# Optimization experiments

Hardware: AMD Instinct MI355X
Metric: run time of the kernel (lower is better)

## Reference

```python
import jax, jax.numpy as jnp
import numpy as np

D1 = 512
D2 = 1024  # = 2*D1 (concat of x1,y1 along channels)
B, S = 4, 2048


def _self_attn(x, Wq, bq, Wk, bk, Wv, bv):
    # Linear layers use torch convention: out = x @ W.T + b
    q = jnp.einsum('bsd,ed->bse', x, Wq) + bq
    k = jnp.einsum('bsd,ed->bse', x, Wk) + bk
    v = jnp.einsum('bsd,ed->bse', x, Wv) + bv
    # NOTE: original module has no 1/sqrt(d) scaling — keep it faithful.
    scores = jnp.einsum('bqe,bke->bqk', q, k)  # [B,S,S]
    attn = jax.nn.softmax(scores, axis=-1)
    return jnp.einsum('bqk,bke->bqe', attn, v)


def setup_inputs() -> dict:
    key = jax.random.key(0)
    ks = jax.random.split(key, 18)
    s1 = 1.0 / np.sqrt(D1)
    s2 = 1.0 / np.sqrt(D2)
    return {
        'x': jax.random.normal(ks[0], (B, S, D1), jnp.float32),
        'y': jax.random.normal(ks[1], (B, S, D1), jnp.float32),
        'sa1_Wq': jax.random.normal(ks[2], (D1, D1), jnp.float32) * s1,
        'sa1_bq': jnp.zeros((D1,), jnp.float32),
        'sa1_Wk': jax.random.normal(ks[3], (D1, D1), jnp.float32) * s1,
        'sa1_bk': jnp.zeros((D1,), jnp.float32),
        'sa1_Wv': jax.random.normal(ks[4], (D1, D1), jnp.float32) * s1,
        'sa1_bv': jnp.zeros((D1,), jnp.float32),
        'sa2_Wq': jax.random.normal(ks[5], (D2, D2), jnp.float32) * s2,
        'sa2_bq': jnp.zeros((D2,), jnp.float32),
        'sa2_Wk': jax.random.normal(ks[6], (D2, D2), jnp.float32) * s2,
        'sa2_bk': jnp.zeros((D2,), jnp.float32),
        'sa2_Wv': jax.random.normal(ks[7], (D2, D2), jnp.float32) * s2,
        'sa2_bv': jnp.zeros((D2,), jnp.float32),
        'weight1': jnp.ones((1,), jnp.float32),
        'weight2': jnp.ones((1,), jnp.float32),
    }


def reference(x, y, sa1_Wq, sa1_bq, sa1_Wk, sa1_bk, sa1_Wv, sa1_bv,
              sa2_Wq, sa2_bq, sa2_Wk, sa2_bk, sa2_Wv, sa2_bv,
              weight1, weight2):
    x1 = _self_attn(x, sa1_Wq, sa1_bq, sa1_Wk, sa1_bk, sa1_Wv, sa1_bv)
    x1 = x1 + y * weight2
    y1 = _self_attn(y, sa1_Wq, sa1_bq, sa1_Wk, sa1_bk, sa1_Wv, sa1_bv)
    y1 = y1 + x * weight1
    temp = jnp.concatenate((x1, y1), axis=2)  # [B,S,2*D1]
    return _self_attn(temp, sa2_Wq, sa2_bq, sa2_Wk, sa2_bk, sa2_Wv, sa2_bv)
```

## Files before the change

### kernel.cpp

```cpp
#include <hip/hip_runtime.h>
#include <hip/hip_bf16.h>
#include <cstdint>
#include <cstddef>


typedef __bf16 bf16;
typedef __attribute__((ext_vector_type(8))) __bf16 bf16x8;
typedef __attribute__((ext_vector_type(4))) __bf16 bf16x4;
typedef __attribute__((ext_vector_type(4))) float f32x4;

__device__ __forceinline__ void gld16(const bf16* g, bf16* s) {
    __builtin_amdgcn_global_load_lds(
        (const __attribute__((address_space(1))) void*)g,
        (__attribute__((address_space(3))) void*)s, 16, 0, 0);
}

#define WAIT_VM8   __builtin_amdgcn_s_waitcnt(8 | (7 << 4) | (0xF << 8))
#define WAIT_VM0   __builtin_amdgcn_s_waitcnt(0 | (7 << 4) | (0xF << 8))
#define WAIT_LGKM0 __builtin_amdgcn_s_waitcnt(0xF | (7 << 4) | (0 << 8) | (3 << 14))

__device__ __forceinline__ int swz(int row, int g) {
    return row * 64 + ((g ^ (row & 7)) << 3);
}

__global__ __launch_bounds__(256) void gemm_split(
    const bf16* __restrict__ A, long lda, long psA, long bsA,
    const bf16* __restrict__ B, long ldb, long psB, long bsB,
    void* __restrict__ C, long ldc, long psC, long bsC, int mode,
    const float* __restrict__ bias, const float* __restrict__ bias2, int nsplit,
    const float* __restrict__ resid, long ldr, long bsR,
    const float* __restrict__ scale,
    int K, int split, int nx, int ny)
{
    __shared__ __align__(16) bf16 As[2][128 * 64];
    __shared__ __align__(16) bf16 Bs[2][128 * 64];

    const int t    = threadIdx.x;
    const int wave = t >> 6;
    const int lane = t & 63;
    const int wr   = wave >> 1;
    const int wc   = wave & 1;
    const int r16  = lane & 15;
    const int quad = lane >> 4;

    const int g    = blockIdx.x;
    const int xcd  = g & 7;
    const int tk   = g >> 3;
    const int nst8 = gridDim.x >> 7;
    const int st   = xcd * nst8 + (tk >> 4);
    const int p    = tk & 15;
    const int snx  = nx >> 2, sny = ny >> 2;
    const int spz  = snx * sny;
    const int zz   = st / spz;
    const int rS   = st - zz * spz;
    const int sy   = rS / snx;
    const int sx   = rS - sy * snx;
    const int yb   = sy * 4 + (p >> 2);
    const int xb   = sx * 4 + (p & 3);
    const long z   = zz;

    const long row0 = (long)yb * 128;
    const long col0 = (long)xb * 128;

    const int srow = (lane >> 3);
    const int scol = ((lane & 7) ^ srow) * 8;

    const int ktiles = K >> 6;
    const int T = split * ktiles;

    const bf16* Az = A + z * bsA;
    const bf16* Bz = B + z * bsB;

    auto prefetch = [&](int ti, int buf) {
        const int ph = ti / ktiles;
        const int kt = (ti - ph * ktiles) << 6;
        const bf16* Ab = Az + (ph == 1 ? psA : 0);
        const bf16* Bb = Bz + (ph == 2 ? psB : 0);
#pragma unroll
        for (int p2 = 0; p2 < 4; ++p2) {
            const int chunk = wave * 32 + p2 * 8;
            gld16(Ab + (row0 + chunk + srow) * lda + kt + scol, &As[buf][chunk * 64]);
            gld16(Bb + (col0 + chunk + srow) * ldb + kt + scol, &Bs[buf][chunk * 64]);
        }
    };

    f32x4 acc[4][4];
#pragma unroll
    for (int r = 0; r < 4; ++r)
#pragma unroll
        for (int c = 0; c < 4; ++c)
            acc[r][c] = (f32x4){0.f, 0.f, 0.f, 0.f};

    prefetch(0, 0);
    prefetch(1, 1);
    for (int ti = 0; ti < T; ++ti) {
        const int cur = ti & 1;
        if (ti + 1 < T) WAIT_VM8; else WAIT_VM0;
        __builtin_amdgcn_s_barrier();
        bf16x8 af[2][4], bg[2][4];
#pragma unroll
        for (int kk = 0; kk < 2; ++kk) {
            const int g0 = (kk << 2) + quad;
#pragma unroll
            for (int r = 0; r < 4; ++r)
                af[kk][r] = *reinterpret_cast<const bf16x8*>(&As[cur][swz(wr * 64 + r * 16 + r16, g0)]);
#pragma unroll
            for (int c = 0; c < 4; ++c)
                bg[kk][c] = *reinterpret_cast<const bf16x8*>(&Bs[cur][swz(wc * 64 + c * 16 + r16, g0)]);
        }
        WAIT_LGKM0;
        __builtin_amdgcn_s_barrier();
        if (ti + 2 < T) prefetch(ti + 2, cur);
#pragma unroll
        for (int kk = 0; kk < 2; ++kk)
#pragma unroll
            for (int r = 0; r < 4; ++r)
#pragma unroll
                for (int c = 0; c < 4; ++c)
                    acc[r][c] = __builtin_amdgcn_mfma_f32_16x16x32_bf16(af[kk][r], bg[kk][c], acc[r][c], 0, 0, 0);
    }

    const float scv = resid ? *scale : 0.f;

#pragma unroll
    for (int r = 0; r < 4; ++r) {
#pragma unroll
        for (int c = 0; c < 4; ++c) {
            long gcol = col0 + wc * 64 + c * 16 + r16;
            float bv = 0.f;
            if (bias) bv = (gcol < nsplit) ? bias[gcol] : bias2[gcol - nsplit];
#pragma unroll
            for (int i = 0; i < 4; ++i) {
                long grow = row0 + wr * 64 + r * 16 + quad * 4 + i;
                float val = acc[r][c][i] + bv;
                if (mode == 0) {
                    if (resid) val += resid[z * bsR + grow * ldr + gcol] * scv;
                    ((float*)C)[z * bsC + grow * ldc + gcol] = val;
                } else if (mode == 1) {
                    if (resid) val += resid[z * bsR + grow * ldr + gcol] * scv;
                    bf16* Cb = (bf16*)C + z * bsC;
                    bf16 h = (bf16)val;
                    Cb[grow * ldc + gcol] = h;
                    Cb[psC + grow * ldc + gcol] = (bf16)(val - (float)h);
                } else {
                    long b = grow >> 11, s = grow & 2047;
                    bf16* Cb = (bf16*)C + b * bsC;
                    bf16 h = (bf16)val;
                    Cb[gcol * ldc + s] = h;
                    Cb[psC + gcol * ldc + s] = (bf16)(val - (float)h);
                }
            }
        }
    }
}

__global__ __launch_bounds__(512) void gemm256(
    const bf16* __restrict__ A, long lda, long psA, long bsA,
    const bf16* __restrict__ B, long ldb, long psB, long bsB,
    void* __restrict__ C, long ldc, long psC, long bsC, int mode,
    const float* __restrict__ bias, const float* __restrict__ bias2, int nsplit,
    int K, int split, int nx, int ny)
{
    __shared__ __align__(16) bf16 As[2][256 * 64];
    __shared__ __align__(16) bf16 Bs[2][256 * 64];

    const int t    = threadIdx.x;
    const int wave = t >> 6;
    const int lane = t & 63;
    const int wm   = wave >> 2;
    const int wn   = wave & 3;
    const int r16  = lane & 15;
    const int quad = lane >> 4;

    const int g     = blockIdx.x;
    const int chunk = gridDim.x >> 3;
    const int idx   = (g & 7) * chunk + (g >> 3);
    const int tpz   = nx * ny;
    const int z     = idx / tpz;
    const int r0i   = idx - z * tpz;
    const int ty    = r0i / nx;
    const int tx    = r0i - ty * nx;
    const long row0 = (long)ty * 256;
    const long col0 = (long)tx * 256;

    const int srow = lane >> 3;
    const int scol = ((lane & 7) ^ srow) * 8;

    const int ktiles = K >> 6;
    const int T = split * ktiles;

    const bf16* Az = A + (long)z * bsA;
    const bf16* Bz = B + (long)z * bsB;

    auto prefetch = [&](int ti, int buf) {
        const int ph = ti / ktiles;
        const int kt = (ti - ph * ktiles) << 6;
        const bf16* Ab = Az + (ph == 1 ? psA : 0);
        const bf16* Bb = Bz + (ph == 2 ? psB : 0);
#pragma unroll
        for (int p2 = 0; p2 < 4; ++p2) {
            const int chnk = wave * 32 + p2 * 8;
            gld16(Ab + (row0 + chnk + srow) * lda + kt + scol, &As[buf][chnk * 64]);
            gld16(Bb + (col0 + chnk + srow) * ldb + kt + scol, &Bs[buf][chnk * 64]);
        }
    };

    f32x4 acc[8][4];
#pragma unroll
    for (int r = 0; r < 8; ++r)
#pragma unroll
        for (int c = 0; c < 4; ++c)
            acc[r][c] = (f32x4){0.f, 0.f, 0.f, 0.f};

    prefetch(0, 0);
    prefetch(1, 1);
    for (int ti = 0; ti < T; ++ti) {
        const int cur = ti & 1;
        if (ti + 1 < T) WAIT_VM8; else WAIT_VM0;
        __builtin_amdgcn_s_barrier();

        bf16x8 afA[4][2], afB[4][2], bg[2][2][2];
#pragma unroll
        for (int kk = 0; kk < 2; ++kk) {
            const int g0 = (kk << 2) + quad;
#pragma unroll
            for (int r = 0; r < 4; ++r)
                afA[r][kk] = *reinterpret_cast<const bf16x8*>(
                    &As[cur][swz(wm * 128 + r * 16 + r16, g0)]);
        }
#pragma unroll
        for (int kk = 0; kk < 2; ++kk) {
            const int g0 = (kk << 2) + quad;
#pragma unroll
            for (int c = 0; c < 2; ++c)
                bg[0][c][kk] = *reinterpret_cast<const bf16x8*>(
                    &Bs[cur][swz(wn * 64 + c * 16 + r16, g0)]);
        }
#pragma unroll
        for (int kk = 0; kk < 2; ++kk) {
            const int g0 = (kk << 2) + quad;
#pragma unroll
            for (int c = 0; c < 2; ++c)
                bg[1][c][kk] = *reinterpret_cast<const bf16x8*>(
                    &Bs[cur][swz(wn * 64 + (2 + c) * 16 + r16, g0)]);
        }
#pragma unroll
        for (int kk = 0; kk < 2; ++kk) {
            const int g0 = (kk << 2) + quad;
#pragma unroll
            for (int r = 0; r < 4; ++r)
                afB[r][kk] = *reinterpret_cast<const bf16x8*>(
                    &As[cur][swz(wm * 128 + (4 + r) * 16 + r16, g0)]);
        }

        __builtin_amdgcn_s_setprio(1);
#pragma unroll
        for (int kk = 0; kk < 2; ++kk)
#pragma unroll
            for (int r = 0; r < 4; ++r)
#pragma unroll
                for (int c = 0; c < 2; ++c)
                    acc[r][c] = __builtin_amdgcn_mfma_f32_16x16x32_bf16(
                        afA[r][kk], bg[0][c][kk], acc[r][c], 0, 0, 0);
#pragma unroll
        for (int kk = 0; kk < 2; ++kk)
#pragma unroll
            for (int r = 0; r < 4; ++r)
#pragma unroll
                for (int c = 0; c < 2; ++c)
                    acc[r][2 + c] = __builtin_amdgcn_mfma_f32_16x16x32_bf16(
                        afA[r][kk], bg[1][c][kk], acc[r][2 + c], 0, 0, 0);
        __builtin_amdgcn_s_setprio(0);

        __builtin_amdgcn_sched_barrier(0);
        WAIT_LGKM0;
        __builtin_amdgcn_s_barrier();
        if (ti + 2 < T) prefetch(ti + 2, cur);

        __builtin_amdgcn_s_setprio(1);
#pragma unroll
        for (int kk = 0; kk < 2; ++kk)
#pragma unroll
            for (int r = 0; r < 4; ++r)
#pragma unroll
                for (int c = 0; c < 2; ++c)
                    acc[4 + r][c] = __builtin_amdgcn_mfma_f32_16x16x32_bf16(
                        afB[r][kk], bg[0][c][kk], acc[4 + r][c], 0, 0, 0);
#pragma unroll
        for (int kk = 0; kk < 2; ++kk)
#pragma unroll
            for (int r = 0; r < 4; ++r)
#pragma unroll
                for (int c = 0; c < 2; ++c)
                    acc[4 + r][2 + c] = __builtin_amdgcn_mfma_f32_16x16x32_bf16(
                        afB[r][kk], bg[1][c][kk], acc[4 + r][2 + c], 0, 0, 0);
        __builtin_amdgcn_s_setprio(0);
    }

#pragma unroll
    for (int r = 0; r < 8; ++r) {
#pragma unroll
        for (int c = 0; c < 4; ++c) {
            const long gcol = col0 + wn * 64 + c * 16 + r16;
            float bv = 0.f;
            if (bias) bv = (gcol < nsplit) ? bias[gcol] : bias2[gcol - nsplit];
#pragma unroll
            for (int i = 0; i < 4; ++i) {
                const long grow = row0 + wm * 128 + r * 16 + quad * 4 + i;
                float val = acc[r][c][i] + bv;
                if (mode == 0) {
                    ((float*)C)[(long)z * bsC + grow * ldc + gcol] = val;
                } else {
                    bf16* Cb = (bf16*)C + (long)z * bsC;
                    bf16 h = (bf16)val;
                    Cb[grow * ldc + gcol] = h;
                    Cb[psC + grow * ldc + gcol] = (bf16)(val - (float)h);
                }
            }
        }
    }
}

__global__ __launch_bounds__(256) void softmax_planes(float* __restrict__ S)
{
    __shared__ float redm[4], reds[4];
    float* srow = S + (long)blockIdx.x * 2048;
    const int t = threadIdx.x;
    const int lane = t & 63;
    const int wave = t >> 6;

    f32x4 v0 = *reinterpret_cast<const f32x4*>(srow + t * 4);
    f32x4 v1 = *reinterpret_cast<const f32x4*>(srow + 1024 + t * 4);

    float m = v0[0];
#pragma unroll
    for (int i = 1; i < 4; ++i) m = fmaxf(m, v0[i]);
#pragma unroll
    for (int i = 0; i < 4; ++i) m = fmaxf(m, v1[i]);
#pragma unroll
    for (int off = 32; off > 0; off >>= 1) m = fmaxf(m, __shfl_xor(m, off));
    if (lane == 0) redm[wave] = m;
    __syncthreads();
    m = fmaxf(fmaxf(redm[0], redm[1]), fmaxf(redm[2], redm[3]));

    float s = 0.f;
#pragma unroll
    for (int i = 0; i < 4; ++i) { v0[i] = __expf(v0[i] - m); s += v0[i]; }
#pragma unroll
    for (int i = 0; i < 4; ++i) { v1[i] = __expf(v1[i] - m); s += v1[i]; }
#pragma unroll
    for (int off = 32; off > 0; off >>= 1) s += __shfl_xor(s, off);
    if (lane == 0) reds[wave] = s;
    __syncthreads();
    s = reds[0] + reds[1] + reds[2] + reds[3];
    float inv = 1.f / s;

    bf16x4 h0, h1, l0, l1;
#pragma unroll
    for (int i = 0; i < 4; ++i) {
        float a = v0[i] * inv, b = v1[i] * inv;
        h0[i] = (bf16)a; l0[i] = (bf16)(a - (float)h0[i]);
        h1[i] = (bf16)b; l1[i] = (bf16)(b - (float)h1[i]);
    }
    bf16* ph = (bf16*)srow;
    *reinterpret_cast<bf16x4*>(ph + t * 4) = h0;
    *reinterpret_cast<bf16x4*>(ph + 1024 + t * 4) = h1;
    *reinterpret_cast<bf16x4*>(ph + 2048 + t * 4) = l0;
    *reinterpret_cast<bf16x4*>(ph + 3072 + t * 4) = l1;
}

__global__ __launch_bounds__(256) void split2_f32(
    const float* __restrict__ in, bf16* __restrict__ hi, bf16* __restrict__ lo)
{
    long i = ((long)blockIdx.x * 256 + threadIdx.x) * 4;
    f32x4 v = *reinterpret_cast<const f32x4*>(in + i);
    bf16x4 h, l;
#pragma unroll
    for (int j = 0; j < 4; ++j) {
        h[j] = (bf16)v[j];
        l[j] = (bf16)(v[j] - (float)h[j]);
    }
    *reinterpret_cast<bf16x4*>(hi + i) = h;
    *reinterpret_cast<bf16x4*>(lo + i) = l;
}

extern "C" void kernel_launch(void* const* d_in, const int* in_sizes, int n_in,
                              void* d_out, int out_size, void* d_ws, size_t ws_size,
                              hipStream_t stream)
{
    const float* x   = (const float*)d_in[0];
    const float* y   = (const float*)d_in[1];
    const float* Wq1 = (const float*)d_in[2];
    const float* bq1 = (const float*)d_in[3];
    const float* Wk1 = (const float*)d_in[4];
    const float* bk1 = (const float*)d_in[5];
    const float* Wv1 = (const float*)d_in[6];
    const float* bv1 = (const float*)d_in[7];
    const float* Wq2 = (const float*)d_in[8];
    const float* bq2 = (const float*)d_in[9];
    const float* Wk2 = (const float*)d_in[10];
    const float* bk2 = (const float*)d_in[11];
    const float* Wv2 = (const float*)d_in[12];
    const float* bv2 = (const float*)d_in[13];
    const float* w1  = (const float*)d_in[14];
    const float* w2  = (const float*)d_in[15];
    float* out = (float*)d_out;

    const size_t MB = 1ull << 20;
    char* ws = (char*)d_ws;
    const long S = 2048, M4 = 8192, E1 = 512, E2 = 1024;
    const long W1ps = E1 * E1, W2ps = E2 * E2;

    const int cfg = (ws_size >= 207 * MB) ? 2 : 0;

    auto gemm = [&](const bf16* A, long lda, long psA, long bsA,
                    const bf16* B, long ldb, long psB, long bsB,
                    void* C, long ldc, long psC, long bsC, int mode,
                    const float* bias, const float* bias2, int nsplit,
                    const float* resid, long ldr, long bsR,
                    const float* scale, int M, int N, int K, int split, int gz) {
        int nx = N / 128, ny = M / 128;
        dim3 g((unsigned)(nx * ny * gz));
        gemm_split<<<g, dim3(256), 0, stream>>>(
            A, lda, psA, bsA, B, ldb, psB, bsB, C, ldc, psC, bsC, mode,
            bias, bias2, nsplit, resid, ldr, bsR, scale, K, split, nx, ny);
    };
    auto g256 = [&](const bf16* A, long lda, long psA, long bsA,
                    const bf16* B, long ldb, long psB, long bsB,
                    void* C, long ldc, long psC, long bsC, int mode,
                    const float* bias, const float* bias2, int nsplit,
                    int K, int split, int M, int N, int gz) {
        int nx = N / 256, ny = M / 256;
        gemm256<<<dim3((unsigned)(nx * ny * gz)), dim3(512), 0, stream>>>(
            A, lda, psA, bsA, B, ldb, psB, bsB, C, ldc, psC, bsC, mode,
            bias, bias2, nsplit, K, split, nx, ny);
    };
    auto conv2 = [&](const float* in, bf16* hi, bf16* lo, long n) {
        split2_f32<<<dim3((unsigned)(n / 1024)), dim3(256), 0, stream>>>(in, hi, lo);
    };

    if (cfg == 2) {
        bf16* xyp   = (bf16*)d_out;
        bf16* Wqk1p = (bf16*)(ws + 0 * MB);
        bf16* Wv1p  = (bf16*)(ws + 2 * MB);
        bf16* Wqk2p = (bf16*)(ws + 3 * MB);
        bf16* Wv2p  = (bf16*)(ws + 11 * MB);
        bf16* temp  = (bf16*)(ws + 15 * MB);
        bf16* qk    = (bf16*)(ws + 47 * MB);
        bf16* vt    = (bf16*)(ws + 111 * MB);
        float* Sc   = (float*)(ws + 143 * MB);

        const long PXY = 16384L * 512;
        const long PW1 = 1024L * 512;
        const long PW2 = 2048L * 1024;
        const long PQ1 = 16384L * 1024;
        const long PQ2 = 8192L * 2048;
        const long PT  = 8192L * 1024;
        const long BV1 = 2 * E1 * S;
        const long BV2 = 2 * E2 * S;

        conv2(x, xyp, xyp + PXY, M4 * E1);
        conv2(y, xyp + M4 * E1, xyp + PXY + M4 * E1, M4 * E1);
        conv2(Wq1, Wqk1p, Wqk1p + PW1, W1ps);
        conv2(Wk1, Wqk1p + W1ps, Wqk1p + PW1 + W1ps, W1ps);
        conv2(Wv1, Wv1p, Wv1p + W1ps, W1ps);
        conv2(Wq2, Wqk2p, Wqk2p + PW2, W2ps);
        conv2(Wk2, Wqk2p + W2ps, Wqk2p + PW2 + W2ps, W2ps);
        conv2(Wv2, Wv2p, Wv2p + W2ps, W2ps);

        g256(xyp, E1, PXY, 0, Wqk1p, E1, PW1, 0,
             qk, 1024, PQ1, 0, 1, bq1, bk1, 512,
             512, 3, 16384, 1024, 1);
        gemm(xyp, E1, PXY, 0, Wv1p, E1, W1ps, 0,
             vt, S, E1 * S, BV1, 2, bv1, nullptr, 512,
             nullptr, 0, 0, nullptr, 16384, 512, 512, 3, 1);

        g256(qk, 1024, PQ1, S * 1024, qk + 512, 1024, PQ1, S * 1024,
             Sc, S, 0, S * S, 0, nullptr, nullptr, 0, 512, 3, 2048, 2048, 4);
        softmax_planes<<<dim3(8192), dim3(256), 0, stream>>>(Sc);
        gemm((const bf16*)Sc, 4096, 2048, S * 4096, vt, S, E1 * S, BV1,
             temp, 1024, PT, S * 1024, 1, nullptr, nullptr, 512,
             y, E1, S * E1, w2, 2048, 512, 2048, 3, 4);

        g256(qk + M4 * 1024, 1024, PQ1, S * 1024,
             qk + M4 * 1024 + 512, 1024, PQ1, S * 1024,
             Sc, S, 0, S * S, 0, nullptr, nullptr, 0, 512, 3, 2048, 2048, 4);
        softmax_planes<<<dim3(8192), dim3(256), 0, stream>>>(Sc);
        gemm((const bf16*)Sc, 4096, 2048, S * 4096, vt + 4 * BV1, S, E1 * S, BV1,
             temp + 512, 1024, PT, S * 1024, 1, nullptr, nullptr, 512,
             x, E1, S * E1, w1, 2048, 512, 2048, 3, 4);

        g256(temp, E2, PT, 0, Wqk2p, E2, PW2, 0,
             qk, 2048, PQ2, 0, 1, bq2, bk2, 1024,
             1024, 3, 8192, 2048, 1);
        gemm(temp, E2, PT, 0, Wv2p, E2, W2ps, 0,
             vt, S, E2 * S, BV2, 2, bv2, nullptr, 1024,
             nullptr, 0, 0, nullptr, 8192, 1024, 1024, 1, 1);
        g256(qk, 2048, PQ2, S * 2048, qk + 1024, 2048, PQ2, S * 2048,
             Sc, S, 0, S * S, 0, nullptr, nullptr, 0, 1024, 3, 2048, 2048, 4);
        softmax_planes<<<dim3(8192), dim3(256), 0, stream>>>(Sc);
        gemm((const bf16*)Sc, 4096, 2048, S * 4096, vt, S, E2 * S, BV2,
             out, E2, 0, S * E2, 0, nullptr, nullptr, 1024,
             nullptr, 0, 0, nullptr, 2048, 1024, 2048, 1, 4);
    } else {
        bf16* xp = (bf16*)d_out;
        bf16* yp = xp + 2 * M4 * E1;
        bf16* Wq1p = (bf16*)(ws + 0 * MB);
        bf16* Wk1p = (bf16*)(ws + 1 * MB);
        bf16* Wv1p = (bf16*)(ws + 2 * MB);
        bf16* temp = (bf16*)(ws + 3 * MB);
        bf16* qb   = (bf16*)(ws + 35 * MB);
        bf16* kb   = (bf16*)(ws + 43 * MB);
        bf16* vt   = (bf16*)(ws + 51 * MB);
        float* Sc  = (float*)(ws + 59 * MB);
        bf16* Wq2p = (bf16*)d_out;
        bf16* Wk2p = Wq2p + 2 * W2ps;
        bf16* Wv2p = Wk2p + 2 * W2ps;

        conv2(x, xp, xp + M4 * E1, M4 * E1);
        conv2(y, yp, yp + M4 * E1, M4 * E1);
        conv2(Wq1, Wq1p, Wq1p + W1ps, W1ps);
        conv2(Wk1, Wk1p, Wk1p + W1ps, W1ps);
        conv2(Wv1, Wv1p, Wv1p + W1ps, W1ps);

        auto stage1 = [&](const bf16* sp, const float* resid, const float* scale, long colOff) {
            for (int b = 0; b < 4; ++b) {
                const bf16* sb = sp + (long)b * S * E1;
                gemm(sb, E1, M4 * E1, 0, Wq1p, E1, W1ps, 0, qb, E1, S * E1, 0, 1,
                     bq1, nullptr, 512, nullptr, 0, 0, nullptr, 2048, 512, 512, 3, 1);
                gemm(sb, E1, M4 * E1, 0, Wk1p, E1, W1ps, 0, kb, E1, S * E1, 0, 1,
                     bk1, nullptr, 512, nullptr, 0, 0, nullptr, 2048, 512, 512, 3, 1);
                gemm(sb, E1, M4 * E1, 0, Wv1p, E1, W1ps, 0, vt, S, E1 * S, 0, 2,
                     bv1, nullptr, 512, nullptr, 0, 0, nullptr, 2048, 512, 512, 3, 1);
                gemm(qb, E1, S * E1, 0, kb, E1, S * E1, 0, Sc, S, 0, 0, 0,
                     nullptr, nullptr, 2048, nullptr, 0, 0, nullptr, 2048, 2048, 512, 3, 1);
                softmax_planes<<<dim3(2048), dim3(256), 0, stream>>>(Sc);
                gemm((const bf16*)Sc, 4096, 2048, 0, vt, S, E1 * S, 0,
                     temp + colOff + (long)b * S * 1024, 1024, M4 * 1024, 0, 1,
                     nullptr, nullptr, 512, resid + (long)b * S * E1, E1, 0, scale,
                     2048, 512, 2048, 3, 1);
            }
        };

        stage1(xp, y, w2, 0);
        stage1(yp, x, w1, 512);

        conv2(Wq2, Wq2p, Wq2p + W2ps, W2ps);
        conv2(Wk2, Wk2p, Wk2p + W2ps, W2ps);
        conv2(Wv2, Wv2p, Wv2p + W2ps, W2ps);

        for (int b = 0; b < 4; ++b) {
            const bf16* tb = temp + (long)b * S * E2;
            gemm(tb, E2, M4 * E2, 0, Wq2p, E2, W2ps, 0, qb, E2, S * E2, 0, 1,
                 bq2, nullptr, 1024, nullptr, 0, 0, nullptr, 2048, 1024, 1024, 3, 1);
            gemm(tb, E2, M4 * E2, 0, Wk2p, E2, W2ps, 0, kb, E2, S * E2, 0, 1,
                 bk2, nullptr, 1024, nullptr, 0, 0, nullptr, 2048, 1024, 1024, 3, 1);
            gemm(tb, E2, M4 * E2, 0, Wv2p, E2, W2ps, 0, vt, S, E2 * S, 0, 2,
                 bv2, nullptr, 1024, nullptr, 0, 0, nullptr, 2048, 1024, 1024, 1, 1);
            gemm(qb, E2, S * E2, 0, kb, E2, S * E2, 0, Sc, S, 0, 0, 0,
                 nullptr, nullptr, 2048, nullptr, 0, 0, nullptr, 2048, 2048, 1024, 3, 1);
            softmax_planes<<<dim3(2048), dim3(256), 0, stream>>>(Sc);
            gemm((const bf16*)Sc, 4096, 2048, 0, vt, S, E2 * S, 0,
                 out + (long)b * S * E2, E2, 0, 0, 0, nullptr, nullptr, 1024,
                 nullptr, 0, 0, nullptr, 2048, 1024, 2048, 1, 1);
        }
    }

    (void)in_sizes; (void)n_in; (void)out_size;
}
```

Measured before the change: 906.1 us.

## Split-K the stage-1 attention PV GEMMs and reduce partials with fused residual

The stage-1 P·V GEMMs (M=2048, N=512 per batch, K=2048) launched only 256 tiles, which underfills the GPU. They are now split along K into two halves, doubling the grid to 512 blocks. Each half writes fp32 partials to scratch in the output buffer through a new mode 3. A new reduce_pv kernel sums the partials, adds the scaled residual and writes the hi/lo bf16 pair into temp. This adds an extra fp32 round trip through memory and one more kernel launch per stage.

```diff
diff --git a/kernel.cpp b/kernel.cpp
--- a/kernel.cpp
+++ b/kernel.cpp
@@ -30,7 +30,7 @@
     const float* __restrict__ bias, const float* __restrict__ bias2, int nsplit,
     const float* __restrict__ resid, long ldr, long bsR,
     const float* __restrict__ scale,
-    int K, int split, int nx, int ny)
+    int K, int split, int nx, int ny, int nz)
 {
     __shared__ __align__(16) bf16 As[2][128 * 64];
     __shared__ __align__(16) bf16 Bs[2][128 * 64];
@@ -57,7 +57,10 @@
     const int sx   = rS - sy * snx;
     const int yb   = sy * 4 + (p >> 2);
     const int xb   = sx * 4 + (p & 3);
-    const long z   = zz;
+
+    const int  kh   = zz / nz;
+    const long z    = zz - (long)kh * nz;
+    const long kOff = (long)kh * K;
 
     const long row0 = (long)yb * 128;
     const long col0 = (long)xb * 128;
@@ -79,8 +82,8 @@
 #pragma unroll
         for (int p2 = 0; p2 < 4; ++p2) {
             const int chunk = wave * 32 + p2 * 8;
-            gld16(Ab + (row0 + chunk + srow) * lda + kt + scol, &As[buf][chunk * 64]);
-            gld16(Bb + (col0 + chunk + srow) * ldb + kt + scol, &Bs[buf][chunk * 64]);
+            gld16(Ab + (row0 + chunk + srow) * lda + kt + kOff + scol, &As[buf][chunk * 64]);
+            gld16(Bb + (col0 + chunk + srow) * ldb + kt + kOff + scol, &Bs[buf][chunk * 64]);
         }
     };
 
@@ -142,6 +145,8 @@
                     bf16 h = (bf16)val;
                     Cb[grow * ldc + gcol] = h;
                     Cb[psC + grow * ldc + gcol] = (bf16)(val - (float)h);
+                } else if (mode == 3) {
+                    ((float*)C)[(long)kh * psC + z * bsC + grow * ldc + gcol] = val;
                 } else {
                     long b = grow >> 11, s = grow & 2047;
                     bf16* Cb = (bf16*)C + b * bsC;
@@ -319,6 +324,33 @@
             }
         }
     }
+}
+
+__global__ __launch_bounds__(256) void reduce_pv(
+    const float* __restrict__ p0, const float* __restrict__ p1,
+    const float* __restrict__ resid, const float* __restrict__ scale,
+    bf16* __restrict__ outp, long psC)
+{
+    const long gid = (long)blockIdx.x * 256 + threadIdx.x;
+    const long f4  = gid * 4;
+    const long z   = f4 >> 20;
+    const long rem = f4 & ((1L << 20) - 1);
+    const long row = rem >> 9;
+    const long col = rem & 511;
+    const float scv = *scale;
+    f32x4 a = *reinterpret_cast<const f32x4*>(p0 + f4);
+    f32x4 b = *reinterpret_cast<const f32x4*>(p1 + f4);
+    f32x4 r = *reinterpret_cast<const f32x4*>(resid + f4);
+    bf16x4 h, l;
+#pragma unroll
+    for (int j = 0; j < 4; ++j) {
+        float v = a[j] + b[j] + r[j] * scv;
+        h[j] = (bf16)v;
+        l[j] = (bf16)(v - (float)h[j]);
+    }
+    bf16* dst = outp + z * (2048L * 1024) + row * 1024 + col;
+    *reinterpret_cast<bf16x4*>(dst) = h;
+    *reinterpret_cast<bf16x4*>(dst + psC) = l;
 }
 
 __global__ __launch_bounds__(256) void softmax_planes(float* __restrict__ S)
@@ -418,12 +450,13 @@
                     void* C, long ldc, long psC, long bsC, int mode,
                     const float* bias, const float* bias2, int nsplit,
                     const float* resid, long ldr, long bsR,
-                    const float* scale, int M, int N, int K, int split, int gz) {
+                    const float* scale, int M, int N, int K, int split,
+                    int gz, int nz) {
         int nx = N / 128, ny = M / 128;
         dim3 g((unsigned)(nx * ny * gz));
         gemm_split<<<g, dim3(256), 0, stream>>>(
             A, lda, psA, bsA, B, ldb, psB, bsB, C, ldc, psC, bsC, mode,
-            bias, bias2, nsplit, resid, ldr, bsR, scale, K, split, nx, ny);
+            bias, bias2, nsplit, resid, ldr, bsR, scale, K, split, nx, ny, nz);
     };
     auto g256 = [&](const bf16* A, long lda, long psA, long bsA,
                     const bf16* B, long ldb, long psB, long bsB,
@@ -458,6 +491,8 @@
         const long PT  = 8192L * 1024;
         const long BV1 = 2 * E1 * S;
         const long BV2 = 2 * E2 * S;
+        const long PVH = 4L * 2048 * 512;
+        float* pvScr = (float*)d_out;
 
         conv2(x, xyp, xyp + PXY, M4 * E1);
         conv2(y, xyp + M4 * E1, xyp + PXY + M4 * E1, M4 * E1);
@@ -473,35 +508,39 @@
              512, 3, 16384, 1024, 1);
         gemm(xyp, E1, PXY, 0, Wv1p, E1, W1ps, 0,
              vt, S, E1 * S, BV1, 2, bv1, nullptr, 512,
-             nullptr, 0, 0, nullptr, 16384, 512, 512, 3, 1);
+             nullptr, 0, 0, nullptr, 16384, 512, 512, 3, 1, 1);
 
         g256(qk, 1024, PQ1, S * 1024, qk + 512, 1024, PQ1, S * 1024,
              Sc, S, 0, S * S, 0, nullptr, nullptr, 0, 512, 3, 2048, 2048, 4);
         softmax_planes<<<dim3(8192), dim3(256), 0, stream>>>(Sc);
         gemm((const bf16*)Sc, 4096, 2048, S * 4096, vt, S, E1 * S, BV1,
-             temp, 1024, PT, S * 1024, 1, nullptr, nullptr, 512,
-             y, E1, S * E1, w2, 2048, 512, 2048, 3, 4);
+             pvScr, 512, PVH, 2048L * 512, 3, nullptr, nullptr, 0,
+             nullptr, 0, 0, nullptr, 2048, 512, 1024, 3, 8, 4);
+        reduce_pv<<<dim3(4096), dim3(256), 0, stream>>>(
+            pvScr, pvScr + PVH, y, w2, temp, PT);
 
         g256(qk + M4 * 1024, 1024, PQ1, S * 1024,
              qk + M4 * 1024 + 512, 1024, PQ1, S * 1024,
              Sc, S, 0, S * S, 0, nullptr, nullptr, 0, 512, 3, 2048, 2048, 4);
         softmax_planes<<<dim3(8192), dim3(256), 0, stream>>>(Sc);
         gemm((const bf16*)Sc, 4096, 2048, S * 4096, vt + 4 * BV1, S, E1 * S, BV1,
-             temp + 512, 1024, PT, S * 1024, 1, nullptr, nullptr, 512,
-             x, E1, S * E1, w1, 2048, 512, 2048, 3, 4);
+             pvScr, 512, PVH, 2048L * 512, 3, nullptr, nullptr, 0,
+             nullptr, 0, 0, nullptr, 2048, 512, 1024, 3, 8, 4);
+        reduce_pv<<<dim3(4096), dim3(256), 0, stream>>>(
+            pvScr, pvScr + PVH, x, w1, temp + 512, PT);
 
         g256(temp, E2, PT, 0, Wqk2p, E2, PW2, 0,
              qk, 2048, PQ2, 0, 1, bq2, bk2, 1024,
              1024, 3, 8192, 2048, 1);
         gemm(temp, E2, PT, 0, Wv2p, E2, W2ps, 0,
              vt, S, E2 * S, BV2, 2, bv2, nullptr, 1024,
-             nullptr, 0, 0, nullptr, 8192, 1024, 1024, 1, 1);
+             nullptr, 0, 0, nullptr, 8192, 1024, 1024, 1, 1, 1);
         g256(qk, 2048, PQ2, S * 2048, qk + 1024, 2048, PQ2, S * 2048,
              Sc, S, 0, S * S, 0, nullptr, nullptr, 0, 1024, 3, 2048, 2048, 4);
         softmax_planes<<<dim3(8192), dim3(256), 0, stream>>>(Sc);
         gemm((const bf16*)Sc, 4096, 2048, S * 4096, vt, S, E2 * S, BV2,
              out, E2, 0, S * E2, 0, nullptr, nullptr, 1024,
-             nullptr, 0, 0, nullptr, 2048, 1024, 2048, 1, 4);
+             nullptr, 0, 0, nullptr, 2048, 1024, 2048, 1, 4, 4);
     } else {
         bf16* xp = (bf16*)d_out;
         bf16* yp = xp + 2 * M4 * E1;
@@ -527,18 +566,18 @@
             for (int b = 0; b < 4; ++b) {
                 const bf16* sb = sp + (long)b * S * E1;
                 gemm(sb, E1, M4 * E1, 0, Wq1p, E1, W1ps, 0, qb, E1, S * E1, 0, 1,
-                     bq1, nullptr, 512, nullptr, 0, 0, nullptr, 2048, 512, 512, 3, 1);
+                     bq1, nullptr, 512, nullptr, 0, 0, nullptr, 2048, 512, 512, 3, 1, 1);
                 gemm(sb, E1, M4 * E1, 0, Wk1p, E1, W1ps, 0, kb, E1, S * E1, 0, 1,
-                     bk1, nullptr, 512, nullptr, 0, 0, nullptr, 2048, 512, 512, 3, 1);
+                     bk1, nullptr, 512, nullptr, 0, 0, nullptr, 2048, 512, 512, 3, 1, 1);
                 gemm(sb, E1, M4 * E1, 0, Wv1p, E1, W1ps, 0, vt, S, E1 * S, 0, 2,
-                     bv1, nullptr, 512, nullptr, 0, 0, nullptr, 2048, 512, 512, 3, 1);
+                     bv1, nullptr, 512, nullptr, 0, 0, nullptr, 2048, 512, 512, 3, 1, 1);
                 gemm(qb, E1, S * E1, 0, kb, E1, S * E1, 0, Sc, S, 0, 0, 0,
-                     nullptr, nullptr, 2048, nullptr, 0, 0, nullptr, 2048, 2048, 512, 3, 1);
+                     nullptr, nullptr, 2048, nullptr, 0, 0, nullptr, 2048, 2048, 512, 3, 1, 1);
                 softmax_planes<<<dim3(2048), dim3(256), 0, stream>>>(Sc);
                 gemm((const bf16*)Sc, 4096, 2048, 0, vt, S, E1 * S, 0,
                      temp + colOff + (long)b * S * 1024, 1024, M4 * 1024, 0, 1,
                      nullptr, nullptr, 512, resid + (long)b * S * E1, E1, 0, scale,
-                     2048, 512, 2048, 3, 1);
+                     2048, 512, 2048, 3, 1, 1);
             }
         };
 
@@ -552,17 +591,17 @@
         for (int b = 0; b < 4; ++b) {
             const bf16* tb = temp + (long)b * S * E2;
             gemm(tb, E2, M4 * E2, 0, Wq2p, E2, W2ps, 0, qb, E2, S * E2, 0, 1,
-                 bq2, nullptr, 1024, nullptr, 0, 0, nullptr, 2048, 1024, 1024, 3, 1);
+                 bq2, nullptr, 1024, nullptr, 0, 0, nullptr, 2048, 1024, 1024, 3, 1, 1);
             gemm(tb, E2, M4 * E2, 0, Wk2p, E2, W2ps, 0, kb, E2, S * E2, 0, 1,
-                 bk2, nullptr, 1024, nullptr, 0, 0, nullptr, 2048, 1024, 1024, 3, 1);
+                 bk2, nullptr, 1024, nullptr, 0, 0, nullptr, 2048, 1024, 1024, 3, 1, 1);
             gemm(tb, E2, M4 * E2, 0, Wv2p, E2, W2ps, 0, vt, S, E2 * S, 0, 2,
-                 bv2, nullptr, 1024, nullptr, 0, 0, nullptr, 2048, 1024, 1024, 1, 1);
+                 bv2, nullptr, 1024, nullptr, 0, 0, nullptr, 2048, 1024, 1024, 1, 1, 1);
             gemm(qb, E2, S * E2, 0, kb, E2, S * E2, 0, Sc, S, 0, 0, 0,
-                 nullptr, nullptr, 2048, nullptr, 0, 0, nullptr, 2048, 2048, 1024, 3, 1);
+                 nullptr, nullptr, 2048, nullptr, 0, 0, nullptr, 2048, 2048, 1024, 3, 1, 1);
             softmax_planes<<<dim3(2048), dim3(256), 0, stream>>>(Sc);
             gemm((const bf16*)Sc, 4096, 2048, 0, vt, S, E2 * S, 0,
                  out + (long)b * S * E2, E2, 0, 0, 0, nullptr, nullptr, 1024,
-                 nullptr, 0, 0, nullptr, 2048, 1024, 2048, 1, 1);
+                 nullptr, 0, 0, nullptr, 2048, 1024, 2048, 1, 1, 1);
         }
     }
 
```

Result: faster. 821.9 us (median of 3 runs) (-9.3%).
